# Kernel optimization log

Measured on AMD Instinct MI355X. Metric: run time of the kernel, lower is better.

Reference implementation:

```python
import jax, jax.numpy as jnp
import numpy as np

B, L, HID = 2, 2048, 2048
H = 16
QL = 1536      # q_lora_rank
KVL = 512      # kv_lora_rank
ROPE = 64      # qk_rope_head_dim
NOPE = 128     # qk_nope_head_dim
VD = 128       # v_head_dim
QKD = NOPE + ROPE
SCALE = QKD ** -0.5
EPS = 1e-5
THETA = 10000.0
SQ = (HID / QL) ** 0.5    # mla_scale_q_lora
SKV = (HID / KVL) ** 0.5  # mla_scale_kv_lora


def rmsnorm(x, w, eps=EPS):
    return x * jax.lax.rsqrt(jnp.mean(x * x, axis=-1, keepdims=True) + eps) * w


def rope_traditional(x, base=THETA):
    # x: [..., L, D]; traditional (interleaved-pair) RoPE, offset 0
    D = x.shape[-1]
    Lx = x.shape[-2]
    freqs = base ** (-jnp.arange(0, D, 2, dtype=jnp.float32) / D)  # [D/2]
    th = jnp.arange(Lx, dtype=jnp.float32)[:, None] * freqs[None, :]  # [L, D/2]
    cos, sin = jnp.cos(th), jnp.sin(th)
    x1, x2 = x[..., 0::2], x[..., 1::2]
    r1 = x1 * cos - x2 * sin
    r2 = x1 * sin + x2 * cos
    return jnp.stack([r1, r2], axis=-1).reshape(x.shape)


def setup_inputs() -> dict:
    key = jax.random.key(0)
    ks = jax.random.split(key, 9)
    s = 0.02
    x = jax.random.normal(ks[0], (B, L, HID), dtype=jnp.float32)
    mask = jnp.tril(jnp.ones((L, L), dtype=bool))[None, None]  # causal [1,1,L,L]
    wq_a = jax.random.normal(ks[1], (QL, HID), dtype=jnp.float32) * s
    q_a_ln_w = jnp.ones((QL,), dtype=jnp.float32)
    wq_b = jax.random.normal(ks[2], (H * QKD, QL), dtype=jnp.float32) * s
    wkv_a = jax.random.normal(ks[3], (KVL + ROPE, HID), dtype=jnp.float32) * s
    kv_a_ln_w = jnp.ones((KVL,), dtype=jnp.float32)
    w_embed_q = jax.random.normal(ks[4], (H, KVL, NOPE), dtype=jnp.float32) * s  # [H,out,in]
    w_unembed = jax.random.normal(ks[5], (H, VD, KVL), dtype=jnp.float32) * s    # [H,out,in]
    wo = jax.random.normal(ks[6], (HID, H * VD), dtype=jnp.float32) * s
    return {"x": x, "mask": mask, "wq_a": wq_a, "q_a_ln_w": q_a_ln_w,
            "wq_b": wq_b, "wkv_a": wkv_a, "kv_a_ln_w": kv_a_ln_w,
            "w_embed_q": w_embed_q, "w_unembed": w_unembed, "wo": wo}


def reference(x, mask, wq_a, q_a_ln_w, wq_b, wkv_a, kv_a_ln_w, w_embed_q, w_unembed, wo):
    b, l, _ = x.shape
    # q LoRA path: q_b(RMSNorm(q_a(x)))
    q = rmsnorm(x @ wq_a.T, q_a_ln_w) @ wq_b.T                # [b,l,H*QKD]
    q = q.reshape(b, l, H, QKD).transpose(0, 2, 1, 3) * SQ    # [b,H,l,QKD]
    q_nope, q_pe = q[..., :NOPE], q[..., NOPE:]
    # compressed kv + shared rope key
    ckv = x @ wkv_a.T                                         # [b,l,KVL+ROPE]
    kv_latent = rmsnorm(ckv[..., :KVL], kv_a_ln_w) * SKV      # [b,l,KVL]
    k_pe = ckv[..., KVL:]                                     # [b,l,ROPE] (single shared head)
    q_pe = rope_traditional(q_pe)
    k_pe = rope_traditional(k_pe)
    # rope scores as additive bias, with boolean mask baked in
    pe = jnp.einsum('bhqd,bkd->bhqk', q_pe * SCALE, k_pe)     # [b,H,l,l]
    pe = jnp.where(mask, pe, jnp.finfo(pe.dtype).min)
    # prefill path: up-project latent per head
    k = jnp.einsum('blk,hkn->bhln', kv_latent, w_embed_q)     # transpose=False: x @ W -> [b,H,l,NOPE]
    v = jnp.einsum('blk,hvk->bhlv', kv_latent, w_unembed)     # x @ W^T -> [b,H,l,VD]
    scores = jnp.einsum('bhqd,bhkd->bhqk', q_nope, k) * SCALE + pe
    attn = jax.nn.softmax(scores, axis=-1)
    out = jnp.einsum('bhqk,bhkv->bhqv', attn, v)              # [b,H,l,VD]
    out = out.transpose(0, 2, 1, 3).reshape(b, l, H * VD)
    return out @ wo.T
```

## Files before the change

### kernel.cpp

```cpp
#include <hip/hip_runtime.h>
#include <hip/hip_bf16.h>

#define B_SZ   2
#define L_SEQ  2048
#define HIDD   2048
#define NH     16
#define QL     1536
#define KVLR   512
#define ROPE_D 64
#define NOPE_D 128
#define VD     128
#define QKD    192

typedef __attribute__((ext_vector_type(8))) __bf16 bf16x8;
typedef __attribute__((ext_vector_type(4))) float  f32x4;
typedef __attribute__((ext_vector_type(8))) unsigned short u16x8;

#if __has_builtin(__builtin_amdgcn_exp2f)
#define EXP2(x) __builtin_amdgcn_exp2f(x)
#else
#define EXP2(x) exp2f(x)
#endif

__device__ __forceinline__ float bf2f(unsigned short u) {
    union { float f; unsigned int i; } x; x.i = ((unsigned int)u) << 16; return x.f;
}
__device__ __forceinline__ unsigned short f2bf(float f) {
    __hip_bfloat16 h = __float2bfloat16(f);
    return *reinterpret_cast<unsigned short*>(&h);
}
__device__ __forceinline__ float finclamp(float v) {
    return fminf(fmaxf(v, -3.3e38f), 3.3e38f);
}

__device__ __forceinline__ void gld_lds16(const __hip_bfloat16* g, __hip_bfloat16* l)
{
    __builtin_amdgcn_global_load_lds(
        (const __attribute__((address_space(1))) unsigned int*)(g),
        (__attribute__((address_space(3))) unsigned int*)(l),
        16, 0, 0);
}

__global__ void detect_fp32(const unsigned short* __restrict__ x, int* __restrict__ flag)
{
    if (threadIdx.x == 0 && blockIdx.x == 0) {
        int c = 0;
        for (int i = 0; i < 128; i++) {
            unsigned e = (x[2 * i] >> 7) & 0xFF;
            if (e > 150 || (e > 0 && e < 100)) c++;
        }
        *flag = (c >= 16) ? 1 : 0;
    }
}

struct ConvDesc {
    const void* src[9];
    __hip_bfloat16* dst[9];
    long long n8[9];
};

__global__ __launch_bounds__(256)
void conv_all(ConvDesc d, const int* __restrict__ flag)
{
    const int seg = blockIdx.y;
    const void* src = d.src[seg];
    __hip_bfloat16* dst = d.dst[seg];
    const long long n8 = d.n8[seg];
    const int isf = *flag;
    long long stride = (long long)gridDim.x * 256;
    for (long long i = (long long)blockIdx.x * 256 + threadIdx.x; i < n8; i += stride) {
        u16x8 o;
        if (isf) {
            const float* s = (const float*)src + i * 8;
            float4 a = *(const float4*)s;
            float4 b = *(const float4*)(s + 4);
            o[0] = f2bf(a.x); o[1] = f2bf(a.y); o[2] = f2bf(a.z); o[3] = f2bf(a.w);
            o[4] = f2bf(b.x); o[5] = f2bf(b.y); o[6] = f2bf(b.z); o[7] = f2bf(b.w);
        } else {
            o = ((const u16x8*)src)[i];
        }
        ((u16x8*)dst)[i] = o;
    }
}

__global__ __launch_bounds__(256)
void gemm_bt(const __hip_bfloat16* __restrict__ A,
             const __hip_bfloat16* __restrict__ Bm,
             void* __restrict__ Cv,
             int M, int N, int K, int lda, int ldb, int ldc,
             float scale,
             int dA, int mA, long long sA,
             int dB, int mB, long long sB, long long sC,
             const int* __restrict__ flagp, int fp32out)
{
    int z = blockIdx.z;
    A  += (long long)((z / dA) % mA) * sA;
    Bm += (long long)((z / dB) % mB) * sB;
    const long long coff = (long long)z * sC;

    __shared__ __hip_bfloat16 As[128 * 32];
    __shared__ __hip_bfloat16 Bs[128 * 32];

    const int tid  = threadIdx.x;
    const int lane = tid & 63;
    const int wid  = tid >> 6;
    const int quad = lane >> 4;
    const int l15  = lane & 15;
    const int wm   = (wid >> 1) * 64;
    const int wn   = (wid & 1) * 64;

    const int m0 = blockIdx.y * 128;
    const int n0 = blockIdx.x * 128;

    const int srow = lane >> 2;
    const int scol = (lane & 3) * 8;

    f32x4 acc[4][4] = {};

    for (int k0 = 0; k0 < K; k0 += 32) {
        __syncthreads();
        for (int i = 0; i < 2; i++) {
            int rbase = wid * 32 + i * 16;
            int r = rbase + srow;
            gld_lds16(A + (long long)(m0 + r) * lda + k0 + scol, &As[rbase * 32]);
            int gn = n0 + r; if (gn >= N) gn = N - 1;
            gld_lds16(Bm + (long long)gn * ldb + k0 + scol, &Bs[rbase * 32]);
        }
        __syncthreads();

        bf16x8 af[4], bfv[4];
        for (int mt = 0; mt < 4; mt++)
            af[mt] = *reinterpret_cast<const bf16x8*>(
                &As[(wm + mt * 16 + l15) * 32 + quad * 8]);
        for (int nt = 0; nt < 4; nt++)
            bfv[nt] = *reinterpret_cast<const bf16x8*>(
                &Bs[(wn + nt * 16 + l15) * 32 + quad * 8]);
        for (int mt = 0; mt < 4; mt++)
            for (int nt = 0; nt < 4; nt++)
                acc[mt][nt] = __builtin_amdgcn_mfma_f32_16x16x32_bf16(
                    af[mt], bfv[nt], acc[mt][nt], 0, 0, 0);
    }

    const int f32o = fp32out && (*flagp);

    for (int mt = 0; mt < 4; mt++) {
        int row = m0 + wm + mt * 16 + quad * 4;
        for (int nt = 0; nt < 4; nt++) {
            int col = n0 + wn + nt * 16 + l15;
            if (col < N) {
                for (int r = 0; r < 4; r++) {
                    float val = finclamp(acc[mt][nt][r] * scale);
                    long long idx = coff + (long long)(row + r) * ldc + col;
                    if (f32o) ((float*)Cv)[idx] = val;
                    else      ((__hip_bfloat16*)Cv)[idx] = __float2bfloat16(val);
                }
            }
        }
    }
}

__global__ __launch_bounds__(256)
void rope_q(__hip_bfloat16* __restrict__ Q)
{
    int row = blockIdx.x;
    int l = row & (L_SEQ - 1);
    int tid = threadIdx.x;
    for (int p = tid; p < NH * 32; p += 256) {
        int h = p >> 5, i = p & 31;
        __hip_bfloat16* base = Q + (long long)row * (NH * QKD) + h * QKD + NOPE_D + 2 * i;
        float freq = exp2f(-(float)i * (13.287712379549449f / 32.0f));
        float th = (float)l * freq;
        float s = __sinf(th), c = __cosf(th);
        float x1 = __bfloat162float(base[0]);
        float x2 = __bfloat162float(base[1]);
        base[0] = __float2bfloat16(finclamp(x1 * c - x2 * s));
        base[1] = __float2bfloat16(finclamp(x1 * s + x2 * c));
    }
}

__global__ __launch_bounds__(256)
void rmsnorm_qa(__hip_bfloat16* __restrict__ X, const __hip_bfloat16* __restrict__ W,
                int ldx)
{
    int row = blockIdx.x;
    __hip_bfloat16* xr = X + (long long)row * ldx;
    int tid = threadIdx.x;
    bool act = tid < (QL / 8);
    float v[8];
    float ss = 0.f;
    if (act) {
        u16x8 raw = *reinterpret_cast<const u16x8*>(xr + tid * 8);
        for (int j = 0; j < 8; j++) {
            v[j] = bf2f(((const unsigned short*)&raw)[j]);
            ss += v[j] * v[j];
        }
    }
    for (int m = 1; m < 64; m <<= 1) ss += __shfl_xor(ss, m, 64);
    __shared__ float ws4[4];
    if ((tid & 63) == 0) ws4[tid >> 6] = ss;
    __syncthreads();
    float tot = ws4[0] + ws4[1] + ws4[2] + ws4[3];
    float inv = rsqrtf(tot / (float)QL + 1e-5f);
    if (act) {
        u16x8 wr = *reinterpret_cast<const u16x8*>(W + tid * 8);
        u16x8 o;
        for (int j = 0; j < 8; j++)
            ((unsigned short*)&o)[j] =
                f2bf(finclamp(v[j] * inv * bf2f(((const unsigned short*)&wr)[j])));
        *reinterpret_cast<u16x8*>(xr + tid * 8) = o;
    }
}

__global__ __launch_bounds__(256)
void kv_norm_rope(const __hip_bfloat16* __restrict__ CQ,
                  const __hip_bfloat16* __restrict__ W,
                  __hip_bfloat16* __restrict__ KVLAT,
                  __hip_bfloat16* __restrict__ KPE)
{
    int row = blockIdx.x * 4 + (threadIdx.x >> 6);
    int l = row & (L_SEQ - 1);
    int t = threadIdx.x & 63;
    const __hip_bfloat16* cr = CQ + (long long)row * 2112;

    float v[8]; float ss = 0.f;
    u16x8 raw = *reinterpret_cast<const u16x8*>(cr + t * 8);
    for (int j = 0; j < 8; j++) {
        v[j] = bf2f(((const unsigned short*)&raw)[j]);
        ss += v[j] * v[j];
    }
    for (int m = 1; m < 64; m <<= 1) ss += __shfl_xor(ss, m, 64);
    float inv = rsqrtf(ss / (float)KVLR + 1e-5f) * 2.0f;
    u16x8 wr = *reinterpret_cast<const u16x8*>(W + t * 8);
    u16x8 o;
    for (int j = 0; j < 8; j++)
        ((unsigned short*)&o)[j] =
            f2bf(finclamp(v[j] * inv * bf2f(((const unsigned short*)&wr)[j])));
    *reinterpret_cast<u16x8*>(KVLAT + (long long)row * KVLR + t * 8) = o;

    if (t < 32) {
        float freq = exp2f(-(float)t * (13.287712379549449f / 32.0f));
        float th = (float)l * freq;
        float s = __sinf(th), c = __cosf(th);
        float x1 = __bfloat162float(cr[512 + 2 * t]);
        float x2 = __bfloat162float(cr[512 + 2 * t + 1]);
        __hip_bfloat16* kp = KPE + (long long)row * 64;
        kp[2 * t]     = __float2bfloat16(finclamp(x1 * c - x2 * s));
        kp[2 * t + 1] = __float2bfloat16(finclamp(x1 * s + x2 * c));
    }
}

__global__ __launch_bounds__(256)
void transpose_embed(const __hip_bfloat16* __restrict__ WE,
                     __hip_bfloat16* __restrict__ WB)
{
    int h = blockIdx.y;
    int k0 = blockIdx.x * 64;
    __shared__ __hip_bfloat16 t[64][136];
    int tid = threadIdx.x;
    for (int it = 0; it < 4; it++) {
        int s = tid + it * 256;
        int k = s >> 4, cg = (s & 15) * 8;
        u16x8 v = *reinterpret_cast<const u16x8*>(
            WE + ((long long)h * KVLR + k0 + k) * NOPE_D + cg);
        *reinterpret_cast<u16x8*>(&t[k][cg]) = v;
    }
    __syncthreads();
    for (int it = 0; it < 4; it++) {
        int s = tid + it * 256;
        int n = s >> 3, kg = (s & 7) * 8;
        u16x8 o;
        for (int j = 0; j < 8; j++)
            ((unsigned short*)&o)[j] = *reinterpret_cast<unsigned short*>(&t[kg + j][n]);
        *reinterpret_cast<u16x8*>(WB + ((long long)h * 128 + n) * KVLR + k0 + kg) = o;
    }
}

__global__ __launch_bounds__(256)
void flash_attn(const __hip_bfloat16* __restrict__ Q,
                const __hip_bfloat16* __restrict__ Kb,
                const __hip_bfloat16* __restrict__ Vt,
                const __hip_bfloat16* __restrict__ KPE,
                __hip_bfloat16* __restrict__ OP,
                float* __restrict__ LP)
{
    const int u = blockIdx.x;
    int c, qt;
    if (u < 32)      { c = 0; qt = 31 - u; }
    else if (u < 56) { c = 1; qt = 31 - (u - 32); }
    else if (u < 72) { c = 2; qt = 31 - (u - 56); }
    else             { c = 3; qt = 31 - (u - 72); }
    const int q0 = qt * 64;
    const int t0 = c * 8;
    const int t1 = (qt + 1 < t0 + 8) ? (qt + 1) : (t0 + 8);

    const int bh = blockIdx.y;
    const int b = bh >> 4;
    const int h = bh & 15;

    __shared__ __hip_bfloat16 Ks[64 * 200];
    __shared__ __hip_bfloat16 Vs[128 * 72];
    __shared__ __hip_bfloat16 Ps[4][16 * 72];

    const int tid  = threadIdx.x;
    const int lane = tid & 63;
    const int w    = tid >> 6;
    const int quad = lane >> 4;
    const int l15  = lane & 15;

    const __hip_bfloat16* Kbh  = Kb + (long long)bh * L_SEQ * 128;
    const __hip_bfloat16* Vth  = Vt + (long long)bh * 128 * L_SEQ;
    const __hip_bfloat16* KPEb = KPE + (long long)b * L_SEQ * 64;

    bf16x8 qf[6];
    {
        long long qoff = (long long)(b * L_SEQ + q0 + w * 16 + l15) * (NH * QKD) + h * QKD;
        for (int kk = 0; kk < 6; kk++)
            qf[kk] = *reinterpret_cast<const bf16x8*>(Q + qoff + kk * 32 + quad * 8);
    }

    f32x4 o_acc[8] = {};
    float l_run[4] = {0.f, 0.f, 0.f, 0.f};

    for (int kt = t0; kt < t1; kt++) {
        const int kk0 = kt * 64;
        const bool partial = (kt == qt);
        __syncthreads();
        for (int it = 0; it < 6; it++) {
            int s = tid + it * 256;
            int r = s / 24, cg = s % 24;
            u16x8 v;
            if (cg < 16)
                v = *reinterpret_cast<const u16x8*>(
                    Kbh + (long long)(kk0 + r) * 128 + cg * 8);
            else
                v = *reinterpret_cast<const u16x8*>(
                    KPEb + (long long)(kk0 + r) * 64 + (cg - 16) * 8);
            *reinterpret_cast<u16x8*>(&Ks[r * 200 + cg * 8]) = v;
        }
        for (int it = 0; it < 4; it++) {
            int s = tid + it * 256;
            int vd = s >> 3, kg = (s & 7) * 8;
            u16x8 v = *reinterpret_cast<const u16x8*>(
                Vth + (long long)vd * L_SEQ + kk0 + kg);
            *reinterpret_cast<u16x8*>(&Vs[vd * 72 + kg]) = v;
        }
        __syncthreads();

        f32x4 sfr[4];
        for (int nt = 0; nt < 4; nt++) {
            f32x4 sacc = {};
            for (int kk = 0; kk < 6; kk++) {
                bf16x8 kf = *reinterpret_cast<const bf16x8*>(
                    &Ks[(nt * 16 + l15) * 200 + kk * 32 + quad * 8]);
                sacc = __builtin_amdgcn_mfma_f32_16x16x32_bf16(qf[kk], kf, sacc, 0, 0, 0);
            }
            sfr[nt] = sacc;
        }

        const int qrow_base = q0 + w * 16 + quad * 4;
        float rs[4] = {0.f, 0.f, 0.f, 0.f};
        if (partial) {
            for (int nt = 0; nt < 4; nt++) {
                int key = kk0 + nt * 16 + l15;
                for (int r = 0; r < 4; r++) {
                    float p = (key > qrow_base + r) ? 0.f : EXP2(sfr[nt][r]);
                    sfr[nt][r] = p;
                    rs[r] += p;
                }
            }
        } else {
            for (int nt = 0; nt < 4; nt++)
                for (int r = 0; r < 4; r++) {
                    float p = EXP2(sfr[nt][r]);
                    sfr[nt][r] = p;
                    rs[r] += p;
                }
        }

        for (int nt = 0; nt < 4; nt++)
            for (int r = 0; r < 4; r++)
                Ps[w][(quad * 4 + r) * 72 + nt * 16 + l15] =
                    __float2bfloat16(sfr[nt][r]);

        for (int r = 0; r < 4; r++) {
            float t = rs[r];
            for (int m = 1; m < 16; m <<= 1) t += __shfl_xor(t, m, 16);
            l_run[r] += t;
        }

        for (int ks = 0; ks < 2; ks++) {
            bf16x8 pf = *reinterpret_cast<const bf16x8*>(
                &Ps[w][l15 * 72 + ks * 32 + quad * 8]);
            for (int vt = 0; vt < 8; vt++) {
                bf16x8 vf = *reinterpret_cast<const bf16x8*>(
                    &Vs[(vt * 16 + l15) * 72 + ks * 32 + quad * 8]);
                o_acc[vt] = __builtin_amdgcn_mfma_f32_16x16x32_bf16(pf, vf, o_acc[vt], 0, 0, 0);
            }
        }
    }

    const int pfx[4] = {0, 4096, 7168, 9216};
    const int orow = q0 + w * 16 + quad * 4;
    const long long rb0 = pfx[c] + (long long)b * (2048 - 512 * c) + (orow - 512 * c);
    for (int r = 0; r < 4; r++) {
        __hip_bfloat16* op = OP + (rb0 + r) * 2048 + h * 128;
        for (int vt = 0; vt < 8; vt++)
            op[vt * 16 + l15] = __float2bfloat16(finclamp(o_acc[vt][r]));
        if (l15 == 0) LP[(rb0 + r) * 16 + h] = l_run[r];
    }
}

__global__ __launch_bounds__(256)
void combine_o(const __hip_bfloat16* __restrict__ OP, const float* __restrict__ LP,
               __hip_bfloat16* __restrict__ aout)
{
    const int row = blockIdx.x;
    const int rl = row & 2047;
    const int b = row >> 11;
    const int nch = (rl >> 9) + 1;
    const int tid = threadIdx.x;
    const int c0 = tid * 8;
    const int h = c0 >> 7;
    const int pfx[4] = {0, 4096, 7168, 9216};

    float acc[8] = {};
    float l = 0.f;
    for (int c = 0; c < nch; c++) {
        long long rb = pfx[c] + (long long)b * (2048 - 512 * c) + (rl - 512 * c);
        l += LP[rb * 16 + h];
        u16x8 v = *reinterpret_cast<const u16x8*>(OP + rb * 2048 + c0);
        for (int j = 0; j < 8; j++)
            acc[j] += bf2f(((const unsigned short*)&v)[j]);
    }
    float inv = 1.0f / fmaxf(l, 1e-30f);
    u16x8 o;
    for (int j = 0; j < 8; j++)
        ((unsigned short*)&o)[j] = f2bf(finclamp(acc[j] * inv));
    *reinterpret_cast<u16x8*>(aout + (long long)row * 2048 + c0) = o;
}

extern "C" void kernel_launch(void* const* d_in, const int* in_sizes, int n_in,
                              void* d_out, int out_size, void* d_ws, size_t ws_size,
                              hipStream_t stream)
{
    const long long want[9] = {
        8388608, 3145728, 1536, 4718592, 1179648, 512, 1048576, 1048576, 4194304
    };
    const void* P[9] = {};
    {
        int j = 0;
        for (int i = 0; i < n_in && j < 9; i++)
            if ((long long)in_sizes[i] == want[j]) P[j++] = d_in[i];
        if (!P[8]) {
            const int map[9] = {0, 2, 3, 4, 5, 6, 7, 8, 9};
            for (int j2 = 0; j2 < 9; j2++) P[j2] = d_in[map[j2]];
        }
    }
    (void)ws_size; (void)out_size;

    char* ws = (char*)d_ws;
    int* flag = (int*)ws;
    char* A = ws + 256;

    __hip_bfloat16* xc     = (__hip_bfloat16*)(A);
    __hip_bfloat16* wfused = (__hip_bfloat16*)(A + 16777216);
    __hip_bfloat16* wqbc   = (__hip_bfloat16*)(A + 25427968);
    __hip_bfloat16* cq     = (__hip_bfloat16*)(A + 34865152);
    __hip_bfloat16* OP = (__hip_bfloat16*)(A);
    float*          LP = (float*)(A + 41943040);

    long long off = 256 + 52166656;
    auto alloc = [&](long long bytes) {
        char* p = ws + off;
        off += ((bytes + 255) / 256) * 256;
        return p;
    };
    __hip_bfloat16* qlnwc  = (__hip_bfloat16*)alloc(3072);
    __hip_bfloat16* kvlnwc = (__hip_bfloat16*)alloc(1024);
    __hip_bfloat16* wembc  = (__hip_bfloat16*)alloc(2097152);
    __hip_bfloat16* wunec  = (__hip_bfloat16*)alloc(2097152);
    __hip_bfloat16* woc    = (__hip_bfloat16*)alloc(8388608);
    __hip_bfloat16* kvl    = (__hip_bfloat16*)alloc(4194304);
    __hip_bfloat16* kpe    = (__hip_bfloat16*)alloc(524288);
    __hip_bfloat16* wBk    = (__hip_bfloat16*)alloc(2097152);
    __hip_bfloat16* kvK    = (__hip_bfloat16*)alloc(16777216);
    __hip_bfloat16* kvVt   = (__hip_bfloat16*)alloc(16777216);
    __hip_bfloat16* qbuf   = (__hip_bfloat16*)alloc(25165824);
    __hip_bfloat16* aout   = (__hip_bfloat16*)alloc(16777216);

    detect_fp32<<<1, 64, 0, stream>>>((const unsigned short*)P[0], flag);
    ConvDesc cd;
    cd.src[0] = P[0]; cd.dst[0] = xc;                  cd.n8[0] = 8388608 / 8;
    cd.src[1] = P[4]; cd.dst[1] = wfused;              cd.n8[1] = 1179648 / 8;
    cd.src[2] = P[1]; cd.dst[2] = wfused + 576LL*2048; cd.n8[2] = 3145728 / 8;
    cd.src[3] = P[2]; cd.dst[3] = qlnwc;               cd.n8[3] = 1536 / 8;
    cd.src[4] = P[3]; cd.dst[4] = wqbc;                cd.n8[4] = 4718592 / 8;
    cd.src[5] = P[5]; cd.dst[5] = kvlnwc;              cd.n8[5] = 512 / 8;
    cd.src[6] = P[6]; cd.dst[6] = wembc;               cd.n8[6] = 1048576 / 8;
    cd.src[7] = P[7]; cd.dst[7] = wunec;               cd.n8[7] = 1048576 / 8;
    cd.src[8] = P[8]; cd.dst[8] = woc;                 cd.n8[8] = 4194304 / 8;
    conv_all<<<dim3(512, 9), 256, 0, stream>>>(cd, flag);

    gemm_bt<<<dim3(17, 32, 1), 256, 0, stream>>>(
        xc, wfused, cq, 4096, 2112, 2048, 2048, 2048, 2112, 1.0f,
        1, 1, 0, 1, 1, 0, 0, flag, 0);
    kv_norm_rope<<<1024, 256, 0, stream>>>(cq, kvlnwc, kvl, kpe);
    transpose_embed<<<dim3(8, 16), 256, 0, stream>>>(wembc, wBk);
    gemm_bt<<<dim3(1, 16, 32), 256, 0, stream>>>(
        kvl, wBk, kvK, 2048, 128, 512, 512, 512, 128, 1.0f,
        16, 2, (long long)L_SEQ * KVLR, 1, 16, 128LL * KVLR,
        (long long)L_SEQ * 128, flag, 0);
    gemm_bt<<<dim3(16, 1, 32), 256, 0, stream>>>(
        wunec, kvl, kvVt, 128, 2048, 512, 512, 512, 2048, 1.0f,
        1, 16, 128LL * KVLR, 16, 2, (long long)L_SEQ * KVLR,
        128LL * L_SEQ, flag, 0);
    rmsnorm_qa<<<4096, 256, 0, stream>>>(cq + 576, qlnwc, 2112);
    gemm_bt<<<dim3(24, 32, 1), 256, 0, stream>>>(
        cq + 576, wqbc, qbuf, 4096, 3072, 1536, 2112, 1536, 3072,
        0.1202245867417521f,
        1, 1, 0, 1, 1, 0, 0, flag, 0);
    rope_q<<<4096, 256, 0, stream>>>(qbuf);
    flash_attn<<<dim3(80, 32), 256, 0, stream>>>(
        qbuf, kvK, kvVt, kpe, OP, LP);
    combine_o<<<4096, 256, 0, stream>>>(OP, LP, aout);
    gemm_bt<<<dim3(16, 32, 1), 256, 0, stream>>>(
        aout, woc, (void*)d_out, 4096, 2048, 2048, 2048, 2048, 2048, 1.0f,
        1, 1, 0, 1, 1, 0, 0, flag, 1);
}
```

Before: 530.7 us.

## Merge prep kernels and batch three independent GEMMs into one launch

Combines kv_norm_rope, rmsnorm_qa and transpose_embed into a single block-partitioned prep3 kernel. It also replaces three separate GEMM launches (q_b projection, K up-projection, V up-projection) with one gemm3 kernel that assigns block ranges to each problem. The aim is to cut launch overhead and let the small K/V GEMMs fill the GPU alongside the larger q GEMM instead of running under-occupied. The combined kernel drops the fp32-output path and shares one tile config across all three GEMMs.

```diff
diff --git a/kernel.cpp b/kernel.cpp
--- a/kernel.cpp
+++ b/kernel.cpp
@@ -159,6 +159,187 @@
     }
 }
 
+struct GP {
+    const __hip_bfloat16* A;
+    const __hip_bfloat16* B;
+    __hip_bfloat16* C;
+    int N, K, lda, ldb, ldc;
+    float scale;
+    int dA, mA; long long sA;
+    int dB, mB; long long sB, sC;
+    int nblk, gx, gxy;
+};
+
+__global__ __launch_bounds__(256)
+void gemm3(GP g0, GP g1, GP g2)
+{
+    GP p; int t;
+    int bid = blockIdx.x;
+    if (bid < g0.nblk)               { p = g0; t = bid; }
+    else if (bid < g0.nblk + g1.nblk){ p = g1; t = bid - g0.nblk; }
+    else                             { p = g2; t = bid - g0.nblk - g1.nblk; }
+    const int lz = t / p.gxy;
+    const int rr2 = t % p.gxy;
+    const int ly = rr2 / p.gx;
+    const int lx = rr2 % p.gx;
+
+    const __hip_bfloat16* A  = p.A + (long long)((lz / p.dA) % p.mA) * p.sA;
+    const __hip_bfloat16* Bm = p.B + (long long)((lz / p.dB) % p.mB) * p.sB;
+    const long long coff = (long long)lz * p.sC;
+    const int N = p.N, K = p.K, lda = p.lda, ldb = p.ldb, ldc = p.ldc;
+
+    __shared__ __hip_bfloat16 As[128 * 32];
+    __shared__ __hip_bfloat16 Bs[128 * 32];
+
+    const int tid  = threadIdx.x;
+    const int lane = tid & 63;
+    const int wid  = tid >> 6;
+    const int quad = lane >> 4;
+    const int l15  = lane & 15;
+    const int wm   = (wid >> 1) * 64;
+    const int wn   = (wid & 1) * 64;
+
+    const int m0 = ly * 128;
+    const int n0 = lx * 128;
+
+    const int srow = lane >> 2;
+    const int scol = (lane & 3) * 8;
+
+    f32x4 acc[4][4] = {};
+
+    for (int k0 = 0; k0 < K; k0 += 32) {
+        __syncthreads();
+        for (int i = 0; i < 2; i++) {
+            int rbase = wid * 32 + i * 16;
+            int r = rbase + srow;
+            gld_lds16(A + (long long)(m0 + r) * lda + k0 + scol, &As[rbase * 32]);
+            int gn = n0 + r; if (gn >= N) gn = N - 1;
+            gld_lds16(Bm + (long long)gn * ldb + k0 + scol, &Bs[rbase * 32]);
+        }
+        __syncthreads();
+
+        bf16x8 af[4], bfv[4];
+        for (int mt = 0; mt < 4; mt++)
+            af[mt] = *reinterpret_cast<const bf16x8*>(
+                &As[(wm + mt * 16 + l15) * 32 + quad * 8]);
+        for (int nt = 0; nt < 4; nt++)
+            bfv[nt] = *reinterpret_cast<const bf16x8*>(
+                &Bs[(wn + nt * 16 + l15) * 32 + quad * 8]);
+        for (int mt = 0; mt < 4; mt++)
+            for (int nt = 0; nt < 4; nt++)
+                acc[mt][nt] = __builtin_amdgcn_mfma_f32_16x16x32_bf16(
+                    af[mt], bfv[nt], acc[mt][nt], 0, 0, 0);
+    }
+
+    __hip_bfloat16* C = p.C;
+    const float scale = p.scale;
+    for (int mt = 0; mt < 4; mt++) {
+        int row = m0 + wm + mt * 16 + quad * 4;
+        for (int nt = 0; nt < 4; nt++) {
+            int col = n0 + wn + nt * 16 + l15;
+            if (col < N) {
+                for (int r = 0; r < 4; r++) {
+                    float val = finclamp(acc[mt][nt][r] * scale);
+                    C[coff + (long long)(row + r) * ldc + col] = __float2bfloat16(val);
+                }
+            }
+        }
+    }
+}
+
+__global__ __launch_bounds__(256)
+void prep3(const __hip_bfloat16* __restrict__ CQ,
+           __hip_bfloat16* __restrict__ CQm,
+           const __hip_bfloat16* __restrict__ KVW,
+           const __hip_bfloat16* __restrict__ QW,
+           const __hip_bfloat16* __restrict__ WE,
+           __hip_bfloat16* __restrict__ KVLAT,
+           __hip_bfloat16* __restrict__ KPE,
+           __hip_bfloat16* __restrict__ WB)
+{
+    __shared__ __hip_bfloat16 tls[64 * 136];
+    const int blk = blockIdx.x;
+    const int tid = threadIdx.x;
+
+    if (blk < 1024) {
+        int row = blk * 4 + (tid >> 6);
+        int l = row & (L_SEQ - 1);
+        int t = tid & 63;
+        const __hip_bfloat16* cr = CQ + (long long)row * 2112;
+        float v[8]; float ss = 0.f;
+        u16x8 raw = *reinterpret_cast<const u16x8*>(cr + t * 8);
+        for (int j = 0; j < 8; j++) {
+            v[j] = bf2f(((const unsigned short*)&raw)[j]);
+            ss += v[j] * v[j];
+        }
+        for (int m = 1; m < 64; m <<= 1) ss += __shfl_xor(ss, m, 64);
+        float inv = rsqrtf(ss / (float)KVLR + 1e-5f) * 2.0f;
+        u16x8 wr = *reinterpret_cast<const u16x8*>(KVW + t * 8);
+        u16x8 o;
+        for (int j = 0; j < 8; j++)
+            ((unsigned short*)&o)[j] =
+                f2bf(finclamp(v[j] * inv * bf2f(((const unsigned short*)&wr)[j])));
+        *reinterpret_cast<u16x8*>(KVLAT + (long long)row * KVLR + t * 8) = o;
+        if (t < 32) {
+            float freq = exp2f(-(float)t * (13.287712379549449f / 32.0f));
+            float th = (float)l * freq;
+            float s = __sinf(th), c = __cosf(th);
+            float x1 = __bfloat162float(cr[512 + 2 * t]);
+            float x2 = __bfloat162float(cr[512 + 2 * t + 1]);
+            __hip_bfloat16* kp = KPE + (long long)row * 64;
+            kp[2 * t]     = __float2bfloat16(finclamp(x1 * c - x2 * s));
+            kp[2 * t + 1] = __float2bfloat16(finclamp(x1 * s + x2 * c));
+        }
+    } else if (blk < 5120) {
+        int row = blk - 1024;
+        __hip_bfloat16* xr = CQm + (long long)row * 2112 + 576;
+        bool act = tid < (QL / 8);
+        float v[8]; float ss = 0.f;
+        if (act) {
+            u16x8 raw = *reinterpret_cast<const u16x8*>(xr + tid * 8);
+            for (int j = 0; j < 8; j++) {
+                v[j] = bf2f(((const unsigned short*)&raw)[j]);
+                ss += v[j] * v[j];
+            }
+        }
+        for (int m = 1; m < 64; m <<= 1) ss += __shfl_xor(ss, m, 64);
+        float* ws4 = (float*)tls;
+        if ((tid & 63) == 0) ws4[tid >> 6] = ss;
+        __syncthreads();
+        float tot = ws4[0] + ws4[1] + ws4[2] + ws4[3];
+        float inv = rsqrtf(tot / (float)QL + 1e-5f);
+        if (act) {
+            u16x8 wr = *reinterpret_cast<const u16x8*>(QW + tid * 8);
+            u16x8 o;
+            for (int j = 0; j < 8; j++)
+                ((unsigned short*)&o)[j] =
+                    f2bf(finclamp(v[j] * inv * bf2f(((const unsigned short*)&wr)[j])));
+            *reinterpret_cast<u16x8*>(xr + tid * 8) = o;
+        }
+    } else {
+        int t = blk - 5120;
+        int h = t >> 3;
+        int k0 = (t & 7) * 64;
+        for (int it = 0; it < 4; it++) {
+            int s = tid + it * 256;
+            int k = s >> 4, cg = (s & 15) * 8;
+            u16x8 v = *reinterpret_cast<const u16x8*>(
+                WE + ((long long)h * KVLR + k0 + k) * NOPE_D + cg);
+            *reinterpret_cast<u16x8*>(&tls[k * 136 + cg]) = v;
+        }
+        __syncthreads();
+        for (int it = 0; it < 4; it++) {
+            int s = tid + it * 256;
+            int n = s >> 3, kg = (s & 7) * 8;
+            u16x8 o;
+            for (int j = 0; j < 8; j++)
+                ((unsigned short*)&o)[j] =
+                    *reinterpret_cast<unsigned short*>(&tls[(kg + j) * 136 + n]);
+            *reinterpret_cast<u16x8*>(WB + ((long long)h * 128 + n) * KVLR + k0 + kg) = o;
+        }
+    }
+}
+
 __global__ __launch_bounds__(256)
 void rope_q(__hip_bfloat16* __restrict__ Q)
 {
@@ -175,103 +356,6 @@
         float x2 = __bfloat162float(base[1]);
         base[0] = __float2bfloat16(finclamp(x1 * c - x2 * s));
         base[1] = __float2bfloat16(finclamp(x1 * s + x2 * c));
-    }
-}
-
-__global__ __launch_bounds__(256)
-void rmsnorm_qa(__hip_bfloat16* __restrict__ X, const __hip_bfloat16* __restrict__ W,
-                int ldx)
-{
-    int row = blockIdx.x;
-    __hip_bfloat16* xr = X + (long long)row * ldx;
-    int tid = threadIdx.x;
-    bool act = tid < (QL / 8);
-    float v[8];
-    float ss = 0.f;
-    if (act) {
-        u16x8 raw = *reinterpret_cast<const u16x8*>(xr + tid * 8);
-        for (int j = 0; j < 8; j++) {
-            v[j] = bf2f(((const unsigned short*)&raw)[j]);
-            ss += v[j] * v[j];
-        }
-    }
-    for (int m = 1; m < 64; m <<= 1) ss += __shfl_xor(ss, m, 64);
-    __shared__ float ws4[4];
-    if ((tid & 63) == 0) ws4[tid >> 6] = ss;
-    __syncthreads();
-    float tot = ws4[0] + ws4[1] + ws4[2] + ws4[3];
-    float inv = rsqrtf(tot / (float)QL + 1e-5f);
-    if (act) {
-        u16x8 wr = *reinterpret_cast<const u16x8*>(W + tid * 8);
-        u16x8 o;
-        for (int j = 0; j < 8; j++)
-            ((unsigned short*)&o)[j] =
-                f2bf(finclamp(v[j] * inv * bf2f(((const unsigned short*)&wr)[j])));
-        *reinterpret_cast<u16x8*>(xr + tid * 8) = o;
-    }
-}
-
-__global__ __launch_bounds__(256)
-void kv_norm_rope(const __hip_bfloat16* __restrict__ CQ,
-                  const __hip_bfloat16* __restrict__ W,
-                  __hip_bfloat16* __restrict__ KVLAT,
-                  __hip_bfloat16* __restrict__ KPE)
-{
-    int row = blockIdx.x * 4 + (threadIdx.x >> 6);
-    int l = row & (L_SEQ - 1);
-    int t = threadIdx.x & 63;
-    const __hip_bfloat16* cr = CQ + (long long)row * 2112;
-
-    float v[8]; float ss = 0.f;
-    u16x8 raw = *reinterpret_cast<const u16x8*>(cr + t * 8);
-    for (int j = 0; j < 8; j++) {
-        v[j] = bf2f(((const unsigned short*)&raw)[j]);
-        ss += v[j] * v[j];
-    }
-    for (int m = 1; m < 64; m <<= 1) ss += __shfl_xor(ss, m, 64);
-    float inv = rsqrtf(ss / (float)KVLR + 1e-5f) * 2.0f;
-    u16x8 wr = *reinterpret_cast<const u16x8*>(W + t * 8);
-    u16x8 o;
-    for (int j = 0; j < 8; j++)
-        ((unsigned short*)&o)[j] =
-            f2bf(finclamp(v[j] * inv * bf2f(((const unsigned short*)&wr)[j])));
-    *reinterpret_cast<u16x8*>(KVLAT + (long long)row * KVLR + t * 8) = o;
-
-    if (t < 32) {
-        float freq = exp2f(-(float)t * (13.287712379549449f / 32.0f));
-        float th = (float)l * freq;
-        float s = __sinf(th), c = __cosf(th);
-        float x1 = __bfloat162float(cr[512 + 2 * t]);
-        float x2 = __bfloat162float(cr[512 + 2 * t + 1]);
-        __hip_bfloat16* kp = KPE + (long long)row * 64;
-        kp[2 * t]     = __float2bfloat16(finclamp(x1 * c - x2 * s));
-        kp[2 * t + 1] = __float2bfloat16(finclamp(x1 * s + x2 * c));
-    }
-}
-
-__global__ __launch_bounds__(256)
-void transpose_embed(const __hip_bfloat16* __restrict__ WE,
-                     __hip_bfloat16* __restrict__ WB)
-{
-    int h = blockIdx.y;
-    int k0 = blockIdx.x * 64;
-    __shared__ __hip_bfloat16 t[64][136];
-    int tid = threadIdx.x;
-    for (int it = 0; it < 4; it++) {
-        int s = tid + it * 256;
-        int k = s >> 4, cg = (s & 15) * 8;
-        u16x8 v = *reinterpret_cast<const u16x8*>(
-            WE + ((long long)h * KVLR + k0 + k) * NOPE_D + cg);
-        *reinterpret_cast<u16x8*>(&t[k][cg]) = v;
-    }
-    __syncthreads();
-    for (int it = 0; it < 4; it++) {
-        int s = tid + it * 256;
-        int n = s >> 3, kg = (s & 7) * 8;
-        u16x8 o;
-        for (int j = 0; j < 8; j++)
-            ((unsigned short*)&o)[j] = *reinterpret_cast<unsigned short*>(&t[kg + j][n]);
-        *reinterpret_cast<u16x8*>(WB + ((long long)h * 128 + n) * KVLR + k0 + kg) = o;
     }
 }
 
@@ -504,21 +588,30 @@
     gemm_bt<<<dim3(17, 32, 1), 256, 0, stream>>>(
         xc, wfused, cq, 4096, 2112, 2048, 2048, 2048, 2112, 1.0f,
         1, 1, 0, 1, 1, 0, 0, flag, 0);
-    kv_norm_rope<<<1024, 256, 0, stream>>>(cq, kvlnwc, kvl, kpe);
-    transpose_embed<<<dim3(8, 16), 256, 0, stream>>>(wembc, wBk);
-    gemm_bt<<<dim3(1, 16, 32), 256, 0, stream>>>(
-        kvl, wBk, kvK, 2048, 128, 512, 512, 512, 128, 1.0f,
-        16, 2, (long long)L_SEQ * KVLR, 1, 16, 128LL * KVLR,
-        (long long)L_SEQ * 128, flag, 0);
-    gemm_bt<<<dim3(16, 1, 32), 256, 0, stream>>>(
-        wunec, kvl, kvVt, 128, 2048, 512, 512, 512, 2048, 1.0f,
-        1, 16, 128LL * KVLR, 16, 2, (long long)L_SEQ * KVLR,
-        128LL * L_SEQ, flag, 0);
-    rmsnorm_qa<<<4096, 256, 0, stream>>>(cq + 576, qlnwc, 2112);
-    gemm_bt<<<dim3(24, 32, 1), 256, 0, stream>>>(
-        cq + 576, wqbc, qbuf, 4096, 3072, 1536, 2112, 1536, 3072,
-        0.1202245867417521f,
-        1, 1, 0, 1, 1, 0, 0, flag, 0);
+    prep3<<<5248, 256, 0, stream>>>(cq, cq, kvlnwc, qlnwc, wembc,
+                                    kvl, kpe, wBk);
+    {
+        GP g0, g1, g2;
+        g0.A = cq + 576; g0.B = wqbc; g0.C = qbuf;
+        g0.N = 3072; g0.K = 1536; g0.lda = 2112; g0.ldb = 1536; g0.ldc = 3072;
+        g0.scale = 0.1202245867417521f;
+        g0.dA = 1; g0.mA = 1; g0.sA = 0;
+        g0.dB = 1; g0.mB = 1; g0.sB = 0; g0.sC = 0;
+        g0.nblk = 768; g0.gx = 24; g0.gxy = 768;
+        g1.A = kvl; g1.B = wBk; g1.C = kvK;
+        g1.N = 128; g1.K = 512; g1.lda = 512; g1.ldb = 512; g1.ldc = 128;
+        g1.scale = 1.0f;
+        g1.dA = 16; g1.mA = 2; g1.sA = (long long)L_SEQ * KVLR;
+        g1.dB = 1; g1.mB = 16; g1.sB = 128LL * KVLR; g1.sC = (long long)L_SEQ * 128;
+        g1.nblk = 512; g1.gx = 1; g1.gxy = 16;
+        g2.A = wunec; g2.B = kvl; g2.C = kvVt;
+        g2.N = 2048; g2.K = 512; g2.lda = 512; g2.ldb = 512; g2.ldc = 2048;
+        g2.scale = 1.0f;
+        g2.dA = 1; g2.mA = 16; g2.sA = 128LL * KVLR;
+        g2.dB = 16; g2.mB = 2; g2.sB = (long long)L_SEQ * KVLR; g2.sC = 128LL * L_SEQ;
+        g2.nblk = 512; g2.gx = 16; g2.gxy = 16;
+        gemm3<<<1792, 256, 0, stream>>>(g0, g1, g2);
+    }
     rope_q<<<4096, 256, 0, stream>>>(qbuf);
     flash_attn<<<dim3(80, 32), 256, 0, stream>>>(
         qbuf, kvK, kvVt, kpe, OP, LP);
```

Result: faster. 499.7 us (-5.9%).
